# Performance work log

Measured on AMD Instinct MI355X. Metric: run time of the kernel, lower is better.

The kernel has to match this reference:

```python
import jax, jax.numpy as jnp
import numpy as np

NEG_INF = -1e9

def setup_inputs() -> dict:
    key = jax.random.key(0)
    ks = jax.random.split(key, 7)
    B, NQ, NK, DQ, DK, DV, DH = 16, 128, 2048, 256, 256, 128, 64
    queries = jax.random.normal(ks[0], (B, NQ, DQ), dtype=jnp.float32)
    keys = jax.random.normal(ks[1], (B, NK, DK), dtype=jnp.float32)
    values = jax.random.normal(ks[2], (B, NK, DV), dtype=jnp.float32)
    valid_lens = jax.random.randint(ks[3], (B,), 1, NK + 1, dtype=jnp.int32)
    Wq = jax.random.normal(ks[4], (DQ, DH), dtype=jnp.float32) / np.sqrt(DQ)
    Wk = jax.random.normal(ks[5], (DK, DH), dtype=jnp.float32) / np.sqrt(DK)
    wv = jax.random.normal(ks[6], (DH,), dtype=jnp.float32) / np.sqrt(DH)
    return {"queries": queries, "keys": keys, "values": values,
            "valid_lens": valid_lens, "Wq": Wq, "Wk": Wk, "wv": wv}


def reference(queries, keys, values, valid_lens, Wq, Wk, wv):
    # Additive (Bahdanau) attention.
    q = jnp.einsum('bqd,dh->bqh', queries, Wq)   # [B, nq, dH]
    k = jnp.einsum('bkd,dh->bkh', keys, Wk)      # [B, nk, dH]
    # broadcast add -> tanh -> reduce with wv: scores [B, nq, nk]
    feat = jnp.tanh(q[:, :, None, :] + k[:, None, :, :])  # [B, nq, nk, dH]
    scores = jnp.einsum('bqkh,h->bqk', feat, wv)
    # masked softmax over nk using per-batch valid lengths
    nk = keys.shape[1]
    mask = jnp.arange(nk)[None, None, :] < valid_lens[:, None, None]  # [B,1,nk]
    scores = jnp.where(mask, scores, NEG_INF)
    attn = jax.nn.softmax(scores, axis=-1)
    # dropout is identity at eval time
    return jnp.einsum('bqk,bkv->bqv', attn, values)  # [B, nq, dv]
```

## Files before the change

### kernel.cpp

```cpp
#include <hip/hip_runtime.h>
#include <stddef.h>


__device__ __forceinline__ float fast_rcp(float x)  { return __builtin_amdgcn_rcpf(x); }
__device__ __forceinline__ float fast_exp2(float x) { return __builtin_amdgcn_exp2f(x); }

#define C2F 2.88539008177792681f
#define L2E 1.44269504088896340f

template<bool TRANSPOSED>
__device__ __forceinline__
void proj_body(const float* __restrict__ inb, const float* __restrict__ W,
               float* __restrict__ out, int b, int r0, int rowsPerB, int t)
{
  __shared__ float4 Wlds[256 * 16];
  __shared__ float  klds[64 * 36];

  const float4* W4 = (const float4*)W;
  #pragma unroll
  for (int i = 0; i < 16; ++i) Wlds[t + 256 * i] = W4[t + 256 * i];

  const int j = t >> 4;
  const int g = t & 15;

  float acc[4][4];
  #pragma unroll
  for (int m = 0; m < 4; ++m)
    acc[m][0] = acc[m][1] = acc[m][2] = acc[m][3] = 0.f;

  for (int dc = 0; dc < 8; ++dc) {
    {
      const int row = t >> 2, cs = (t & 3) * 8;
      const float* s = inb + row * 256 + dc * 32 + cs;
      float4 a0 = *(const float4*)s;
      float4 a1 = *(const float4*)(s + 4);
      float* dst = &klds[row * 36 + cs];
      *(float4*)dst       = a0;
      *(float4*)(dst + 4) = a1;
    }
    __syncthreads();
    #pragma unroll
    for (int d = 0; d < 32; ++d) {
      float4 w4 = Wlds[(dc * 32 + d) * 16 + j];
      #pragma unroll
      for (int m = 0; m < 4; ++m) {
        float kv = klds[(g + 16 * m) * 36 + d];
        acc[m][0] = fmaf(kv, w4.x, acc[m][0]);
        acc[m][1] = fmaf(kv, w4.y, acc[m][1]);
        acc[m][2] = fmaf(kv, w4.z, acc[m][2]);
        acc[m][3] = fmaf(kv, w4.w, acc[m][3]);
      }
    }
    __syncthreads();
  }

  if constexpr (TRANSPOSED) {
    #pragma unroll
    for (int m = 0; m < 4; ++m) {
      int k = r0 + g + 16 * m;
      size_t base = ((size_t)(b * 16 + (k >> 7)) * 64) * 128 + (k & 127);
      #pragma unroll
      for (int i = 0; i < 4; ++i)
        out[base + (size_t)(4 * j + i) * 128] = fast_exp2(C2F * acc[m][i]);
    }
  } else {
    #pragma unroll
    for (int m = 0; m < 4; ++m) {
      int row = r0 + g + 16 * m;
      float4 o;
      o.x = fast_exp2(C2F * acc[m][0]);
      o.y = fast_exp2(C2F * acc[m][1]);
      o.z = fast_exp2(C2F * acc[m][2]);
      o.w = fast_exp2(C2F * acc[m][3]);
      *(float4*)&out[((size_t)b * rowsPerB + row) * 64 + 4 * j] = o;
    }
  }
}

__global__ __launch_bounds__(256)
void proj_qk_kernel(const float* __restrict__ queries, const float* __restrict__ keys,
                    const float* __restrict__ Wq, const float* __restrict__ Wk,
                    float* __restrict__ Eq, float* __restrict__ Ek,
                    const int* __restrict__ vlens)
{
  const int blk = blockIdx.x;
  const bool isq = blk >= 512;
  const int idx = isq ? blk - 512 : blk;
  const int b   = idx & 15;
  const int rt  = idx >> 4;
  const int r0  = rt * 64;
  if (!isq && r0 >= vlens[b]) return;

  const float* in  = isq ? queries : keys;
  const float* W   = isq ? Wq : Wk;
  float* out       = isq ? Eq : Ek;
  const int rowsPerB = isq ? 128 : 2048;
  proj_body<false>(in + ((size_t)b * rowsPerB + r0) * 256, W, out, b, r0, rowsPerB,
                   threadIdx.x);
}

template<bool TRANSPOSED, bool CHECK>
__global__ __launch_bounds__(256)
void proj_kernel(const float* __restrict__ in, const float* __restrict__ W,
                 float* __restrict__ out, const int* __restrict__ vlens,
                 int rowsPerB)
{
  const int t  = threadIdx.x;
  const int b  = blockIdx.x & 15;
  const int rt = blockIdx.x >> 4;
  const int r0 = rt * 64;
  if constexpr (CHECK) {
    if (r0 >= vlens[b]) return;
  }
  proj_body<TRANSPOSED>(in + ((size_t)b * rowsPerB + r0) * 256, W, out, b, r0,
                        rowsPerB, t);
}

__global__ __launch_bounds__(256, 4)
void scorepv_kernel(const float* __restrict__ Eq, const float* __restrict__ Ek,
                    const float* __restrict__ values, const int* __restrict__ vlens,
                    const float* __restrict__ wv,
                    float* __restrict__ partial, float* __restrict__ tsum)
{
  const int blk = blockIdx.x;
  const int g   = blk >> 3;
  const int qq  = blk & 7;
  const int kt  = g >> 4;
  const int b   = g & 15;
  const int vl  = vlens[b];
  if (kt * 128 >= vl) return;

  __shared__ float ek_lds[64 * 128];

  const int t = threadIdx.x;

  {
    const float4* src = (const float4*)(Ek + ((size_t)(b * 2048 + kt * 128)) * 64);
    #pragma unroll
    for (int i = 0; i < 4; ++i) {
      int u   = t + 256 * i;
      int kp2 = u & 63;
      int hq  = u >> 6;
      float4 a0 = src[(2 * kp2) * 16 + hq];
      float4 a1 = src[(2 * kp2 + 1) * 16 + hq];
      *(float2*)&ek_lds[(4 * hq + 0) * 128 + 2 * kp2] = make_float2(a0.x, a1.x);
      *(float2*)&ek_lds[(4 * hq + 1) * 128 + 2 * kp2] = make_float2(a0.y, a1.y);
      *(float2*)&ek_lds[(4 * hq + 2) * 128 + 2 * kp2] = make_float2(a0.z, a1.z);
      *(float2*)&ek_lds[(4 * hq + 3) * 128 + 2 * kp2] = make_float2(a0.w, a1.w);
    }
  }

  float w0 = 0.f, W1 = 0.f;
  #pragma unroll
  for (int u = 0; u < 16; ++u) {
    float4 v = ((const float4*)wv)[u];
    w0 += v.x + v.y + v.z + v.w;
    W1 += fabsf(v.x) + fabsf(v.y) + fabsf(v.z) + fabsf(v.w);
  }

  __syncthreads();

  const int wave_u = __builtin_amdgcn_readfirstlane(t >> 6);
  const int lane   = t & 63;
  const int q0g    = qq * 16 + wave_u * 4;
  const int kp     = lane * 2;
  const float* eqb = Eq + (size_t)(b * 128 + q0g) * 64;

  float s[4][2];
  #pragma unroll
  for (int q = 0; q < 4; ++q) { s[q][0] = w0; s[q][1] = w0; }

  #pragma unroll 4
  for (int hp = 0; hp < 32; ++hp) {
    float2 ekA = *(const float2*)&ek_lds[(2 * hp) * 128 + kp];
    float2 ekB = *(const float2*)&ek_lds[(2 * hp + 1) * 128 + kp];
    float2 wvp = *(const float2*)&wv[2 * hp];
    float wa = -2.0f * wvp.x, wb = -2.0f * wvp.y;
    #pragma unroll
    for (int q = 0; q < 4; ++q) {
      float2 eqp = *(const float2*)&eqb[q * 64 + 2 * hp];
      {
        float x0 = fmaf(eqp.x, ekA.x, 1.f);
        float x1 = fmaf(eqp.y, ekB.x, 1.f);
        float y  = fast_rcp(x0 * x1);
        float a  = wb * x0;
        a = fmaf(wa, x1, a);
        s[q][0] = fmaf(a, y, s[q][0]);
      }
      {
        float x0 = fmaf(eqp.x, ekA.y, 1.f);
        float x1 = fmaf(eqp.y, ekB.y, 1.f);
        float y  = fast_rcp(x0 * x1);
        float a  = wb * x0;
        a = fmaf(wa, x1, a);
        s[q][1] = fmaf(a, y, s[q][1]);
      }
    }
  }

  const int kbase = kt * 128 + kp;
  float p[4][2];
  #pragma unroll
  for (int q = 0; q < 4; ++q) {
    p[q][0] = (kbase     < vl) ? fast_exp2((s[q][0] - W1) * L2E) : 0.f;
    p[q][1] = (kbase + 1 < vl) ? fast_exp2((s[q][1] - W1) * L2E) : 0.f;
  }

  #pragma unroll
  for (int q = 0; q < 4; ++q) {
    float e = p[q][0] + p[q][1];
    #pragma unroll
    for (int m = 1; m < 64; m <<= 1) e += __shfl_xor(e, m, 64);
    if (lane == 0) tsum[(size_t)(b * 16 + kt) * 128 + q0g + q] = e;
  }

  __syncthreads();
  float* p_lds = ek_lds;
  const int q0l = wave_u * 4;
  *(float4*)&p_lds[kp * 20 + q0l]       = make_float4(p[0][0], p[1][0], p[2][0], p[3][0]);
  *(float4*)&p_lds[(kp + 1) * 20 + q0l] = make_float4(p[0][1], p[1][1], p[2][1], p[3][1]);
  __syncthreads();

  const int kg = t >> 7, v = t & 127;
  const int kloc = min(128, vl - kt * 128);
  const int k0 = kg * 64, k1 = min(k0 + 64, kloc);
  const float* vb = values + ((size_t)(b * 2048 + kt * 128)) * 128 + v;
  float acc[16];
  #pragma unroll
  for (int i = 0; i < 16; ++i) acc[i] = 0.f;

  #pragma unroll 4
  for (int k = k0; k < k1; ++k) {
    float vx = vb[(size_t)k * 128];
    const float* pr = &p_lds[k * 20];
    float4 p0 = *(const float4*)&pr[0];
    float4 p1 = *(const float4*)&pr[4];
    float4 p2 = *(const float4*)&pr[8];
    float4 p3 = *(const float4*)&pr[12];
    acc[ 0] = fmaf(p0.x, vx, acc[ 0]); acc[ 1] = fmaf(p0.y, vx, acc[ 1]);
    acc[ 2] = fmaf(p0.z, vx, acc[ 2]); acc[ 3] = fmaf(p0.w, vx, acc[ 3]);
    acc[ 4] = fmaf(p1.x, vx, acc[ 4]); acc[ 5] = fmaf(p1.y, vx, acc[ 5]);
    acc[ 6] = fmaf(p1.z, vx, acc[ 6]); acc[ 7] = fmaf(p1.w, vx, acc[ 7]);
    acc[ 8] = fmaf(p2.x, vx, acc[ 8]); acc[ 9] = fmaf(p2.y, vx, acc[ 9]);
    acc[10] = fmaf(p2.z, vx, acc[10]); acc[11] = fmaf(p2.w, vx, acc[11]);
    acc[12] = fmaf(p3.x, vx, acc[12]); acc[13] = fmaf(p3.y, vx, acc[13]);
    acc[14] = fmaf(p3.z, vx, acc[14]); acc[15] = fmaf(p3.w, vx, acc[15]);
  }

  float* red = ek_lds + 128 * 20;
  if (kg == 1) {
    #pragma unroll
    for (int q = 0; q < 16; ++q) red[q * 128 + v] = acc[q];
  }
  __syncthreads();
  if (kg == 0) {
    #pragma unroll
    for (int q = 0; q < 16; ++q) {
      float tot = acc[q] + red[q * 128 + v];
      partial[(((size_t)(b * 128 + qq * 16 + q)) * 16 + kt) * 128 + v] = tot;
    }
  }
}

__global__ __launch_bounds__(256)
void reduce_kernel(const float* __restrict__ partial, const float* __restrict__ tsum,
                   const int* __restrict__ vlens, float* __restrict__ out)
{
  const int blk = blockIdx.x;
  const int b   = blk >> 6;
  const int q   = (blk & 63) * 2 + (threadIdx.x >> 7);
  const int v   = threadIdx.x & 127;
  const int ntk = (vlens[b] + 127) >> 7;

  float tot = 0.f;
  for (int i = 0; i < ntk; ++i)
    tot += tsum[(size_t)(b * 16 + i) * 128 + q];

  float acc = 0.f;
  const float* pp = partial + ((size_t)(b * 128 + q)) * 16 * 128 + v;
  for (int i = 0; i < ntk; ++i)
    acc += pp[(size_t)i * 128];

  out[((size_t)(b * 128 + q)) * 128 + v] = acc / tot;
}

__global__ __launch_bounds__(256)
void attn_kernel(const float* __restrict__ Eq, const float* __restrict__ EkT,
                 const float* __restrict__ values, const int* __restrict__ vlens,
                 const float* __restrict__ wv, float* __restrict__ out)
{
  const int t    = threadIdx.x;
  const int b    = blockIdx.x & 15;
  const int qt   = blockIdx.x >> 4;
  const int wave = t >> 6;
  const int lane = t & 63;

  __shared__ float4 sc4[512 * 4];
  __shared__ float  pvp[128 * 5];
  __shared__ float  linvs[4];

  const int vl = vlens[b];

  float eqv[64], wv2[64];
  float w0 = 0.f;
  {
    const float4* eq4 = (const float4*)(Eq + (size_t)(b * 128 + qt * 4 + wave) * 64);
    const float4* wv4 = (const float4*)wv;
    #pragma unroll
    for (int u = 0; u < 16; ++u) {
      float4 e = eq4[u], v = wv4[u];
      eqv[4*u+0] = e.x; eqv[4*u+1] = e.y; eqv[4*u+2] = e.z; eqv[4*u+3] = e.w;
      wv2[4*u+0] = -2.f * v.x; wv2[4*u+1] = -2.f * v.y;
      wv2[4*u+2] = -2.f * v.z; wv2[4*u+3] = -2.f * v.w;
      w0 += v.x + v.y + v.z + v.w;
    }
  }

  const int ktiles = (vl + 127) >> 7;
  const int kp = 2 * lane;
  for (int kt = 0; kt < ktiles; ++kt) {
    const float* tb = EkT + ((size_t)(b * 16 + kt) * 64) * 128 + kp;
    float s0 = w0, s1 = w0;
    #pragma unroll
    for (int h = 0; h < 64; ++h) {
      float2 ek = *(const float2*)(tb + (size_t)h * 128);
      float r0 = fast_rcp(fmaf(eqv[h], ek.x, 1.0f));
      float r1 = fast_rcp(fmaf(eqv[h], ek.y, 1.0f));
      s0 = fmaf(wv2[h], r0, s0);
      s1 = fmaf(wv2[h], r1, s1);
    }
    int k = kt * 128 + kp;
    if (k     >= vl) s0 = -1e9f;
    if (k + 1 >= vl) s1 = -1e9f;
    float* scf = (float*)sc4;
    *(float2*)(scf + (((k >> 2) * 4 + wave) * 4 + (k & 3))) = make_float2(s0, s1);
  }

  const int nq4 = (vl + 3) >> 2;
  float mx = -3e38f;
  for (int Q = lane; Q < nq4; Q += 64) {
    float4 f = sc4[Q * 4 + wave];
    mx = fmaxf(mx, fmaxf(fmaxf(f.x, f.y), fmaxf(f.z, f.w)));
  }
  #pragma unroll
  for (int msk = 1; msk < 64; msk <<= 1) mx = fmaxf(mx, __shfl_xor(mx, msk, 64));
  float lsum = 0.f;
  for (int Q = lane; Q < nq4; Q += 64) {
    float4 f = sc4[Q * 4 + wave];
    f.x = fast_exp2((f.x - mx) * L2E);
    f.y = fast_exp2((f.y - mx) * L2E);
    f.z = fast_exp2((f.z - mx) * L2E);
    f.w = fast_exp2((f.w - mx) * L2E);
    sc4[Q * 4 + wave] = f;
    lsum += f.x + f.y + f.z + f.w;
  }
  #pragma unroll
  for (int msk = 1; msk < 64; msk <<= 1) lsum += __shfl_xor(lsum, msk, 64);
  if (lane == 0) linvs[wave] = fast_rcp(lsum);
  __syncthreads();

  const int grp = t >> 7, v = t & 127;
  float acc[4] = {0.f, 0.f, 0.f, 0.f};
  const float* vb = values + (size_t)b * 2048 * 128 + v;
  for (int Q = grp; Q < nq4; Q += 2) {
    float4 p0 = sc4[Q * 4 + 0], p1 = sc4[Q * 4 + 1];
    float4 p2 = sc4[Q * 4 + 2], p3 = sc4[Q * 4 + 3];
    const float* vk = vb + (size_t)(Q * 4) * 128;
    float x;
    x = vk[0];
    acc[0]=fmaf(p0.x,x,acc[0]); acc[1]=fmaf(p1.x,x,acc[1]);
    acc[2]=fmaf(p2.x,x,acc[2]); acc[3]=fmaf(p3.x,x,acc[3]);
    x = vk[128];
    acc[0]=fmaf(p0.y,x,acc[0]); acc[1]=fmaf(p1.y,x,acc[1]);
    acc[2]=fmaf(p2.y,x,acc[2]); acc[3]=fmaf(p3.y,x,acc[3]);
    x = vk[256];
    acc[0]=fmaf(p0.z,x,acc[0]); acc[1]=fmaf(p1.z,x,acc[1]);
    acc[2]=fmaf(p2.z,x,acc[2]); acc[3]=fmaf(p3.z,x,acc[3]);
    x = vk[384];
    acc[0]=fmaf(p0.w,x,acc[0]); acc[1]=fmaf(p1.w,x,acc[1]);
    acc[2]=fmaf(p2.w,x,acc[2]); acc[3]=fmaf(p3.w,x,acc[3]);
  }
  if (grp == 1) {
    #pragma unroll
    for (int qq = 0; qq < 4; ++qq) pvp[v * 5 + qq] = acc[qq];
  }
  __syncthreads();
  if (grp == 0) {
    #pragma unroll
    for (int qq = 0; qq < 4; ++qq) {
      float tot = acc[qq] + pvp[v * 5 + qq];
      out[((size_t)(b * 128) + qt * 4 + qq) * 128 + v] = tot * linvs[qq];
    }
  }
}

extern "C" void kernel_launch(void* const* d_in, const int* in_sizes, int n_in,
                              void* d_out, int out_size, void* d_ws, size_t ws_size,
                              hipStream_t stream) {
  const float* queries = (const float*)d_in[0];
  const float* keys    = (const float*)d_in[1];
  const float* values  = (const float*)d_in[2];
  const int*   vlens   = (const int*)d_in[3];
  const float* Wq      = (const float*)d_in[4];
  const float* Wk      = (const float*)d_in[5];
  const float* wv      = (const float*)d_in[6];
  float* outp = (float*)d_out;

  float* base    = (float*)d_ws;
  float* Eq      = base;
  float* Ek      = base + 131072;
  float* tsumb   = base + 2228224;
  float* partial = base + 2260992;
  const size_t need = (size_t)(2260992 + 4194304) * 4;

  if (ws_size >= need) {
    hipLaunchKernelGGL(proj_qk_kernel, dim3(544), dim3(256), 0, stream,
                       queries, keys, Wq, Wk, Eq, Ek, vlens);
    hipLaunchKernelGGL(scorepv_kernel, dim3(2048), dim3(256), 0, stream,
                       Eq, Ek, values, vlens, wv, partial, tsumb);
    hipLaunchKernelGGL(reduce_kernel, dim3(1024), dim3(256), 0, stream,
                       partial, tsumb, vlens, outp);
  } else {
    hipLaunchKernelGGL((proj_kernel<false, false>), dim3(32), dim3(256), 0, stream,
                       queries, Wq, Eq, (const int*)nullptr, 128);
    hipLaunchKernelGGL((proj_kernel<true, true>), dim3(512), dim3(256), 0, stream,
                       keys, Wk, Ek, vlens, 2048);
    hipLaunchKernelGGL(attn_kernel, dim3(512), dim3(256), 0, stream,
                       Eq, Ek, values, vlens, wv, outp);
  }
}
```

Measured before the change: 84.57 us.

## Pre-pack Ek tiles in projection and double scorepv block to 512 threads

The key projection now writes Ek directly in a per-128-key tile layout matching the score kernel's LDS layout. The score kernel can then fill LDS with a plain float4 copy instead of a transposing gather, and read its operands as one float4 per step. The score/PV kernel is relaunched with 512 threads per block (8 waves of 2 queries each), and the PV loop is split four ways over keys with batched value loads and a three-way LDS reduction. This adds more per-block synchronisation and a larger reduction, and the launch bounds change may increase register pressure.

```diff
diff --git a/kernel.cpp b/kernel.cpp
--- a/kernel.cpp
+++ b/kernel.cpp
@@ -8,7 +8,7 @@
 #define C2F 2.88539008177792681f
 #define L2E 1.44269504088896340f
 
-template<bool TRANSPOSED>
+template<int MODE>
 __device__ __forceinline__
 void proj_body(const float* __restrict__ inb, const float* __restrict__ W,
                float* __restrict__ out, int b, int r0, int rowsPerB, int t)
@@ -54,7 +54,7 @@
     __syncthreads();
   }
 
-  if constexpr (TRANSPOSED) {
+  if constexpr (MODE == 1) {
     #pragma unroll
     for (int m = 0; m < 4; ++m) {
       int k = r0 + g + 16 * m;
@@ -62,6 +62,18 @@
       #pragma unroll
       for (int i = 0; i < 4; ++i)
         out[base + (size_t)(4 * j + i) * 128] = fast_exp2(C2F * acc[m][i]);
+    }
+  } else if constexpr (MODE == 2) {
+    #pragma unroll
+    for (int m = 0; m < 4; ++m) {
+      int k = r0 + g + 16 * m;
+      size_t base = (size_t)(b * 16 + (k >> 7)) * 8192 + (size_t)(k & 127) * 2;
+      float e0 = fast_exp2(C2F * acc[m][0]);
+      float e1 = fast_exp2(C2F * acc[m][1]);
+      float e2 = fast_exp2(C2F * acc[m][2]);
+      float e3 = fast_exp2(C2F * acc[m][3]);
+      *(float2*)&out[base + (size_t)(2 * j) * 256]     = make_float2(e0, e1);
+      *(float2*)&out[base + (size_t)(2 * j + 1) * 256] = make_float2(e2, e3);
     }
   } else {
     #pragma unroll
@@ -80,26 +92,24 @@
 __global__ __launch_bounds__(256)
 void proj_qk_kernel(const float* __restrict__ queries, const float* __restrict__ keys,
                     const float* __restrict__ Wq, const float* __restrict__ Wk,
-                    float* __restrict__ Eq, float* __restrict__ Ek,
+                    float* __restrict__ Eq, float* __restrict__ EkP,
                     const int* __restrict__ vlens)
 {
   const int blk = blockIdx.x;
-  const bool isq = blk >= 512;
-  const int idx = isq ? blk - 512 : blk;
-  const int b   = idx & 15;
-  const int rt  = idx >> 4;
-  const int r0  = rt * 64;
-  if (!isq && r0 >= vlens[b]) return;
-
-  const float* in  = isq ? queries : keys;
-  const float* W   = isq ? Wq : Wk;
-  float* out       = isq ? Eq : Ek;
-  const int rowsPerB = isq ? 128 : 2048;
-  proj_body<false>(in + ((size_t)b * rowsPerB + r0) * 256, W, out, b, r0, rowsPerB,
-                   threadIdx.x);
-}
-
-template<bool TRANSPOSED, bool CHECK>
+  if (blk >= 512) {
+    const int idx = blk - 512;
+    const int b = idx & 15, rt = idx >> 4, r0 = rt * 64;
+    proj_body<0>(queries + ((size_t)b * 128 + r0) * 256, Wq, Eq, b, r0, 128,
+                 threadIdx.x);
+  } else {
+    const int b = blk & 15, rt = blk >> 4, r0 = rt * 64;
+    if (r0 >= vlens[b]) return;
+    proj_body<2>(keys + ((size_t)b * 2048 + r0) * 256, Wk, EkP, b, r0, 2048,
+                 threadIdx.x);
+  }
+}
+
+template<int MODE, bool CHECK>
 __global__ __launch_bounds__(256)
 void proj_kernel(const float* __restrict__ in, const float* __restrict__ W,
                  float* __restrict__ out, const int* __restrict__ vlens,
@@ -112,12 +122,12 @@
   if constexpr (CHECK) {
     if (r0 >= vlens[b]) return;
   }
-  proj_body<TRANSPOSED>(in + ((size_t)b * rowsPerB + r0) * 256, W, out, b, r0,
-                        rowsPerB, t);
-}
-
-__global__ __launch_bounds__(256, 4)
-void scorepv_kernel(const float* __restrict__ Eq, const float* __restrict__ Ek,
+  proj_body<MODE>(in + ((size_t)b * rowsPerB + r0) * 256, W, out, b, r0,
+                  rowsPerB, t);
+}
+
+__global__ __launch_bounds__(512, 6)
+void scorepv_kernel(const float* __restrict__ Eq, const float* __restrict__ EkP,
                     const float* __restrict__ values, const int* __restrict__ vlens,
                     const float* __restrict__ wv,
                     float* __restrict__ partial, float* __restrict__ tsum)
@@ -135,19 +145,10 @@
   const int t = threadIdx.x;
 
   {
-    const float4* src = (const float4*)(Ek + ((size_t)(b * 2048 + kt * 128)) * 64);
-    #pragma unroll
-    for (int i = 0; i < 4; ++i) {
-      int u   = t + 256 * i;
-      int kp2 = u & 63;
-      int hq  = u >> 6;
-      float4 a0 = src[(2 * kp2) * 16 + hq];
-      float4 a1 = src[(2 * kp2 + 1) * 16 + hq];
-      *(float2*)&ek_lds[(4 * hq + 0) * 128 + 2 * kp2] = make_float2(a0.x, a1.x);
-      *(float2*)&ek_lds[(4 * hq + 1) * 128 + 2 * kp2] = make_float2(a0.y, a1.y);
-      *(float2*)&ek_lds[(4 * hq + 2) * 128 + 2 * kp2] = make_float2(a0.z, a1.z);
-      *(float2*)&ek_lds[(4 * hq + 3) * 128 + 2 * kp2] = make_float2(a0.w, a1.w);
-    }
+    const float4* src = (const float4*)(EkP + (size_t)(b * 16 + kt) * 8192);
+    float4* dst = (float4*)ek_lds;
+    #pragma unroll
+    for (int i = 0; i < 4; ++i) dst[t + 512 * i] = src[t + 512 * i];
   }
 
   float w0 = 0.f, W1 = 0.f;
@@ -162,52 +163,42 @@
 
   const int wave_u = __builtin_amdgcn_readfirstlane(t >> 6);
   const int lane   = t & 63;
-  const int q0g    = qq * 16 + wave_u * 4;
+  const int q0g    = qq * 16 + wave_u * 2;
   const int kp     = lane * 2;
   const float* eqb = Eq + (size_t)(b * 128 + q0g) * 64;
 
-  float s[4][2];
-  #pragma unroll
-  for (int q = 0; q < 4; ++q) { s[q][0] = w0; s[q][1] = w0; }
-
-  #pragma unroll 4
+  float s[2][2] = {{w0, w0}, {w0, w0}};
+
+  const float4* ek4 = (const float4*)ek_lds;
+  #pragma unroll 8
   for (int hp = 0; hp < 32; ++hp) {
-    float2 ekA = *(const float2*)&ek_lds[(2 * hp) * 128 + kp];
-    float2 ekB = *(const float2*)&ek_lds[(2 * hp + 1) * 128 + kp];
+    float4 e = ek4[hp * 64 + lane];
     float2 wvp = *(const float2*)&wv[2 * hp];
     float wa = -2.0f * wvp.x, wb = -2.0f * wvp.y;
     #pragma unroll
-    for (int q = 0; q < 4; ++q) {
+    for (int q = 0; q < 2; ++q) {
       float2 eqp = *(const float2*)&eqb[q * 64 + 2 * hp];
-      {
-        float x0 = fmaf(eqp.x, ekA.x, 1.f);
-        float x1 = fmaf(eqp.y, ekB.x, 1.f);
-        float y  = fast_rcp(x0 * x1);
-        float a  = wb * x0;
-        a = fmaf(wa, x1, a);
-        s[q][0] = fmaf(a, y, s[q][0]);
-      }
-      {
-        float x0 = fmaf(eqp.x, ekA.y, 1.f);
-        float x1 = fmaf(eqp.y, ekB.y, 1.f);
-        float y  = fast_rcp(x0 * x1);
-        float a  = wb * x0;
-        a = fmaf(wa, x1, a);
-        s[q][1] = fmaf(a, y, s[q][1]);
-      }
+      { float x0 = fmaf(eqp.x, e.x, 1.f), x1 = fmaf(eqp.y, e.y, 1.f);
+        float y = fast_rcp(x0 * x1);
+        float a = wb * x0; a = fmaf(wa, x1, a);
+        s[q][0] = fmaf(a, y, s[q][0]); }
+      { float x0 = fmaf(eqp.x, e.z, 1.f), x1 = fmaf(eqp.y, e.w, 1.f);
+        float y = fast_rcp(x0 * x1);
+        float a = wb * x0; a = fmaf(wa, x1, a);
+        s[q][1] = fmaf(a, y, s[q][1]); }
     }
   }
 
   const int kbase = kt * 128 + kp;
-  float p[4][2];
-  #pragma unroll
-  for (int q = 0; q < 4; ++q) {
+  float p[2][2];
+  #pragma unroll
+  for (int q = 0; q < 2; ++q) {
     p[q][0] = (kbase     < vl) ? fast_exp2((s[q][0] - W1) * L2E) : 0.f;
     p[q][1] = (kbase + 1 < vl) ? fast_exp2((s[q][1] - W1) * L2E) : 0.f;
   }
 
   #pragma unroll
-  for (int q = 0; q < 4; ++q) {
+  for (int q = 0; q < 2; ++q) {
     float e = p[q][0] + p[q][1];
     #pragma unroll
     for (int m = 1; m < 64; m <<= 1) e += __shfl_xor(e, m, 64);
@@ -216,47 +207,62 @@
 
   __syncthreads();
   float* p_lds = ek_lds;
-  const int q0l = wave_u * 4;
-  *(float4*)&p_lds[kp * 20 + q0l]       = make_float4(p[0][0], p[1][0], p[2][0], p[3][0]);
-  *(float4*)&p_lds[(kp + 1) * 20 + q0l] = make_float4(p[0][1], p[1][1], p[2][1], p[3][1]);
+  const int q0l = wave_u * 2;
+  *(float2*)&p_lds[kp * 20 + q0l]       = make_float2(p[0][0], p[1][0]);
+  *(float2*)&p_lds[(kp + 1) * 20 + q0l] = make_float2(p[0][1], p[1][1]);
   __syncthreads();
 
   const int kg = t >> 7, v = t & 127;
   const int kloc = min(128, vl - kt * 128);
-  const int k0 = kg * 64, k1 = min(k0 + 64, kloc);
+  const int k0 = kg * 32, k1 = min(k0 + 32, kloc);
+  const int len = (k1 > k0) ? (k1 - k0) : 0;
+  const int nfull = len & ~7;
   const float* vb = values + ((size_t)(b * 2048 + kt * 128)) * 128 + v;
   float acc[16];
   #pragma unroll
   for (int i = 0; i < 16; ++i) acc[i] = 0.f;
 
-  #pragma unroll 4
-  for (int k = k0; k < k1; ++k) {
+  for (int kb = k0; kb < k0 + nfull; kb += 8) {
+    float vv[8];
+    #pragma unroll
+    for (int j = 0; j < 8; ++j) vv[j] = vb[(size_t)(kb + j) * 128];
+    #pragma unroll
+    for (int j = 0; j < 8; ++j) {
+      const float* pr = &p_lds[(kb + j) * 20];
+      float4 p0 = *(const float4*)&pr[0];
+      float4 p1 = *(const float4*)&pr[4];
+      float4 p2 = *(const float4*)&pr[8];
+      float4 p3 = *(const float4*)&pr[12];
+      float vx = vv[j];
+      acc[ 0]=fmaf(p0.x,vx,acc[ 0]); acc[ 1]=fmaf(p0.y,vx,acc[ 1]);
+      acc[ 2]=fmaf(p0.z,vx,acc[ 2]); acc[ 3]=fmaf(p0.w,vx,acc[ 3]);
+      acc[ 4]=fmaf(p1.x,vx,acc[ 4]); acc[ 5]=fmaf(p1.y,vx,acc[ 5]);
+      acc[ 6]=fmaf(p1.z,vx,acc[ 6]); acc[ 7]=fmaf(p1.w,vx,acc[ 7]);
+      acc[ 8]=fmaf(p2.x,vx,acc[ 8]); acc[ 9]=fmaf(p2.y,vx,acc[ 9]);
+      acc[10]=fmaf(p2.z,vx,acc[10]); acc[11]=fmaf(p2.w,vx,acc[11]);
+      acc[12]=fmaf(p3.x,vx,acc[12]); acc[13]=fmaf(p3.y,vx,acc[13]);
+      acc[14]=fmaf(p3.z,vx,acc[14]); acc[15]=fmaf(p3.w,vx,acc[15]);
+    }
+  }
+  for (int k = k0 + nfull; k < k1; ++k) {
     float vx = vb[(size_t)k * 128];
     const float* pr = &p_lds[k * 20];
-    float4 p0 = *(const float4*)&pr[0];
-    float4 p1 = *(const float4*)&pr[4];
-    float4 p2 = *(const float4*)&pr[8];
-    float4 p3 = *(const float4*)&pr[12];
-    acc[ 0] = fmaf(p0.x, vx, acc[ 0]); acc[ 1] = fmaf(p0.y, vx, acc[ 1]);
-    acc[ 2] = fmaf(p0.z, vx, acc[ 2]); acc[ 3] = fmaf(p0.w, vx, acc[ 3]);
-    acc[ 4] = fmaf(p1.x, vx, acc[ 4]); acc[ 5] = fmaf(p1.y, vx, acc[ 5]);
-    acc[ 6] = fmaf(p1.z, vx, acc[ 6]); acc[ 7] = fmaf(p1.w, vx, acc[ 7]);
-    acc[ 8] = fmaf(p2.x, vx, acc[ 8]); acc[ 9] = fmaf(p2.y, vx, acc[ 9]);
-    acc[10] = fmaf(p2.z, vx, acc[10]); acc[11] = fmaf(p2.w, vx, acc[11]);
-    acc[12] = fmaf(p3.x, vx, acc[12]); acc[13] = fmaf(p3.y, vx, acc[13]);
-    acc[14] = fmaf(p3.z, vx, acc[14]); acc[15] = fmaf(p3.w, vx, acc[15]);
-  }
-
-  float* red = ek_lds + 128 * 20;
-  if (kg == 1) {
-    #pragma unroll
-    for (int q = 0; q < 16; ++q) red[q * 128 + v] = acc[q];
+    #pragma unroll
+    for (int q = 0; q < 16; ++q) acc[q] = fmaf(pr[q], vx, acc[q]);
+  }
+
+  __syncthreads();
+  float* red = ek_lds;
+  if (kg > 0) {
+    #pragma unroll
+    for (int q = 0; q < 16; ++q) red[(kg - 1) * 2048 + q * 128 + v] = acc[q];
   }
   __syncthreads();
   if (kg == 0) {
     #pragma unroll
     for (int q = 0; q < 16; ++q) {
-      float tot = acc[q] + red[q * 128 + v];
+      float tot = acc[q] + red[q * 128 + v] + red[2048 + q * 128 + v]
+                + red[4096 + q * 128 + v];
       partial[(((size_t)(b * 128 + qq * 16 + q)) * 16 + kt) * 128 + v] = tot;
     }
   }
@@ -408,24 +414,24 @@
 
   float* base    = (float*)d_ws;
   float* Eq      = base;
-  float* Ek      = base + 131072;
+  float* EkP     = base + 131072;
   float* tsumb   = base + 2228224;
   float* partial = base + 2260992;
   const size_t need = (size_t)(2260992 + 4194304) * 4;
 
   if (ws_size >= need) {
     hipLaunchKernelGGL(proj_qk_kernel, dim3(544), dim3(256), 0, stream,
-                       queries, keys, Wq, Wk, Eq, Ek, vlens);
-    hipLaunchKernelGGL(scorepv_kernel, dim3(2048), dim3(256), 0, stream,
-                       Eq, Ek, values, vlens, wv, partial, tsumb);
+                       queries, keys, Wq, Wk, Eq, EkP, vlens);
+    hipLaunchKernelGGL(scorepv_kernel, dim3(2048), dim3(512), 0, stream,
+                       Eq, EkP, values, vlens, wv, partial, tsumb);
     hipLaunchKernelGGL(reduce_kernel, dim3(1024), dim3(256), 0, stream,
                        partial, tsumb, vlens, outp);
   } else {
-    hipLaunchKernelGGL((proj_kernel<false, false>), dim3(32), dim3(256), 0, stream,
+    hipLaunchKernelGGL((proj_kernel<0, false>), dim3(32), dim3(256), 0, stream,
                        queries, Wq, Eq, (const int*)nullptr, 128);
-    hipLaunchKernelGGL((proj_kernel<true, true>), dim3(512), dim3(256), 0, stream,
-                       keys, Wk, Ek, vlens, 2048);
+    hipLaunchKernelGGL((proj_kernel<1, true>), dim3(512), dim3(256), 0, stream,
+                       keys, Wk, EkP, vlens, 2048);
     hipLaunchKernelGGL(attn_kernel, dim3(512), dim3(256), 0, stream,
-                       Eq, Ek, values, vlens, wv, outp);
-  }
-}
+                       Eq, EkP, values, vlens, wv, outp);
+  }
+}
```

Result: slower. 91.24 us (+7.9%).
